# Performance work log

Measured on AMD Instinct MI355X. Metric: run time of the kernel, lower is better.

The kernel has to match this reference:

```python
import jax, jax.numpy as jnp
import numpy as np


def _construct_adj(adj, weight_cross_time):
    # adj: (N, N); weight_cross_time: (S-1, N, N) -> local_adj: (S*N, S*N)
    N = adj.shape[0]
    S = weight_cross_time.shape[0] + 1
    local_adj = jnp.zeros((S * N, S * N), dtype=adj.dtype)
    for i in range(S):  # diagonal blocks (small fixed loop over strides)
        local_adj = local_adj.at[i * N:(i + 1) * N, i * N:(i + 1) * N].set(adj)
    for k in range(S - 1):  # cross-time blocks, symmetric placement
        wk = weight_cross_time[k]
        local_adj = local_adj.at[k * N:(k + 1) * N, (k + 1) * N:(k + 2) * N].set(wk)
        local_adj = local_adj.at[(k + 1) * N:(k + 2) * N, k * N:(k + 1) * N].set(wk.T)
    return local_adj


def setup_inputs() -> dict:
    key = jax.random.key(0)
    k1, k2, k3, k4 = jax.random.split(key, 4)
    N, S, B, Cin, Cout = 1024, 3, 32, 64, 64
    # xavier_uniform-like scales for the learned adjacency parameters
    s_adj = float(np.sqrt(6.0 / (N + N)))
    x = jax.random.normal(k1, (S * N, B, Cin), dtype=jnp.float32)
    adj = jax.random.uniform(k2, (N, N), dtype=jnp.float32, minval=-s_adj, maxval=s_adj)
    weight_cross_time = jax.random.uniform(k3, (S - 1, N, N), dtype=jnp.float32, minval=-s_adj, maxval=s_adj)
    s_fc = float(np.sqrt(1.0 / Cin))
    W = jax.random.uniform(k4, (Cin, 2 * Cout), dtype=jnp.float32, minval=-s_fc, maxval=s_fc)
    b = jnp.zeros((2 * Cout,), dtype=jnp.float32)
    return {"x": x, "adj": adj, "weight_cross_time": weight_cross_time, "W": W, "b": b}


def reference(x, adj, weight_cross_time, W, b):
    # Faithful translation of gcn_operation.forward with activation='GLU'.
    Cout = W.shape[-1] // 2
    local_adj = _construct_adj(adj, weight_cross_time)          # (S*N, S*N)
    h = jnp.einsum('nm,mbc->nbc', local_adj, x)                  # (S*N, B, Cin)
    lhs_rhs = h @ W + b                                          # (S*N, B, 2*Cout)
    lhs, rhs = lhs_rhs[..., :Cout], lhs_rhs[..., Cout:]
    return lhs * jax.nn.sigmoid(rhs)                             # (S*N, B, Cout)
```

## Files before the change

### kernel.cpp

```cpp
#include <hip/hip_runtime.h>

typedef unsigned short u16;
typedef unsigned int   u32;
typedef __attribute__((ext_vector_type(8))) short short8;
typedef __attribute__((ext_vector_type(4))) float f32x4;

__device__ __forceinline__ u16 f2bf(float f) {
    u32 u = __float_as_uint(f);
    u = (u + 0x7fffu + ((u >> 16) & 1u)) >> 16;
    return (u16)u;
}

__device__ __forceinline__ void gld_lds16(const void* g, void* l) {
    __builtin_amdgcn_global_load_lds(
        (const __attribute__((address_space(1))) u32*)g,
        (__attribute__((address_space(3))) u32*)l, 16, 0, 0);
}

__global__ __launch_bounds__(256) void prep_kernel(
    const float* __restrict__ x, const float* __restrict__ adj,
    const float* __restrict__ wct, const float* __restrict__ W,
    u16* __restrict__ Ab, u16* __restrict__ W0T, u16* __restrict__ W1T,
    u16* __restrict__ Xt, u16* __restrict__ Wt)
{
    __shared__ float tile[64][65];
    const int t = threadIdx.x;
    const int bid = blockIdx.x;

    if (bid < 3072) {
        const int i4 = bid * 256 + t;
        const float4 v = (i4 < 262144) ? ((const float4*)adj)[i4]
                                       : ((const float4*)wct)[i4 - 262144];
        ushort4 o;
        o.x = f2bf(v.x); o.y = f2bf(v.y); o.z = f2bf(v.z); o.w = f2bf(v.w);
        ((ushort4*)Ab)[i4] = o;
        return;
    }

    const float* src; u16* dst; int C, R, r0, c0;
    if (bid < 3328)      { const int q = bid - 3072; src = wct;           dst = W0T; C = 1024; R = 1024; r0 = (q & 15) << 6; c0 = (q >> 4) << 6; }
    else if (bid < 3584) { const int q = bid - 3328; src = wct + 1048576; dst = W1T; C = 1024; R = 1024; r0 = (q & 15) << 6; c0 = (q >> 4) << 6; }
    else if (bid < 5120) { const int q = bid - 3584; src = x;             dst = Xt;  C = 2048; R = 3072; r0 = (q % 48) << 6; c0 = (q / 48) << 6; }
    else                 { const int q = bid - 5120; src = W;             dst = Wt;  C = 128;  R = 64;   r0 = 0;             c0 = q << 6; }

#pragma unroll
    for (int it = 0; it < 4; ++it) {
        const int f4 = it * 256 + t;
        const int r  = f4 >> 4;
        const int c4 = (f4 & 15) << 2;
        const float4 v = *(const float4*)&src[(size_t)(r0 + r) * C + c0 + c4];
        tile[r][c4]     = v.x; tile[r][c4 + 1] = v.y;
        tile[r][c4 + 2] = v.z; tile[r][c4 + 3] = v.w;
    }
    __syncthreads();
#pragma unroll
    for (int it = 0; it < 4; ++it) {
        const int f4 = it * 256 + t;
        const int u  = f4 >> 4;
        const int v4 = (f4 & 15) << 2;
        ushort4 o;
        o.x = f2bf(tile[v4][u]);     o.y = f2bf(tile[v4 + 1][u]);
        o.z = f2bf(tile[v4 + 2][u]); o.w = f2bf(tile[v4 + 3][u]);
        *(ushort4*)&dst[(size_t)(c0 + u) * R + r0 + v4] = o;
    }
}

__global__ __launch_bounds__(256, 3) void gemm_h_kernel(
    const u16* __restrict__ Ab,  const u16* __restrict__ W0b,
    const u16* __restrict__ W1b, const u16* __restrict__ W0T,
    const u16* __restrict__ W1T, const u16* __restrict__ Xt,
    const u16* __restrict__ Wt,  const float* __restrict__ bias,
    float* __restrict__ out)
{
    __shared__ u16 Adb[8192];
    __shared__ u16 Bdb[16384];
    __shared__ float Bias_sm[128];

    const int tid = threadIdx.x;
    const int bid = blockIdx.x;
    const int xcd = bid & 7;
    const int idx = bid >> 3;
    const int i   = idx >> 5;
    const int idp = idx & 31;
    const int row0 = (idp & 15) << 6;
    const int nt   = xcd * 2 + (idp >> 4);
    const int col0 = nt << 7;

    const int l    = tid & 63;
    const int w    = tid >> 6;
    const int wr   = ((tid >> 7) & 1) << 5;
    const int wc   = ((tid >> 6) & 1) << 6;
    const int lrow = l & 15;
    const int g16  = l >> 4;
    const int rsw  = lrow & 7;

    const int sub  = tid >> 3;
    const int srck = ((tid & 7) ^ (sub & 7)) << 3;
    const int wofs = w << 9;

    if (tid < 128) Bias_sm[tid] = bias[tid];

    u16 *Ac = Adb, *Ap = Adb + 4096, *Bc = Bdb, *Bp = Bdb + 8192;
    f32x4 acc[2][4] = {};

    auto stageA = [&](u16* dst, const u16* ta, int kel) {
        const u16* ga = ta + (size_t)sub * 1024 + kel + srck;
        gld_lds16(ga,             dst + wofs);
        gld_lds16(ga + 32 * 1024, dst + wofs + 2048);
    };
    auto stageB = [&](u16* dst, const u16* tb, int kel) {
        const u16* gb = tb + (size_t)sub * 3072 + kel + srck;
        gld_lds16(gb,             dst + wofs);
        gld_lds16(gb + 32 * 3072, dst + wofs + 2048);
        gld_lds16(gb + 64 * 3072, dst + wofs + 4096);
        gld_lds16(gb + 96 * 3072, dst + wofs + 6144);
    };
    auto step = [&](const u16* pfa, const u16* pfb, int kel, int do_pf) {
        __builtin_amdgcn_s_barrier();
        if (do_pf) {
            stageA(Ap, pfa, kel);
            stageB(Bp, pfb, kel);
            asm volatile("s_waitcnt vmcnt(6)" ::: "memory");
        } else {
            asm volatile("s_waitcnt vmcnt(0)" ::: "memory");
        }
        __builtin_amdgcn_s_barrier();

        short8 af[2][2], bfr[2][4];
#pragma unroll
        for (int kk = 0; kk < 2; ++kk) {
            const int so = (((kk << 2) | g16) ^ rsw) << 3;
#pragma unroll
            for (int fm = 0; fm < 2; ++fm)
                af[kk][fm] = *(const short8*)&Ac[(wr + fm * 16 + lrow) * 64 + so];
#pragma unroll
            for (int fn = 0; fn < 4; ++fn)
                bfr[kk][fn] = *(const short8*)&Bc[(wc + fn * 16 + lrow) * 64 + so];
        }
#pragma unroll
        for (int kk = 0; kk < 2; ++kk)
#pragma unroll
            for (int fm = 0; fm < 2; ++fm)
#pragma unroll
                for (int fn = 0; fn < 4; ++fn)
                    acc[fm][fn] = __builtin_amdgcn_mfma_f32_16x16x32_bf16(
                        af[kk][fm], bfr[kk][fn], acc[fm][fn], 0, 0, 0);
        u16* t;
        t = Ac; Ac = Ap; Ap = t;
        t = Bc; Bc = Bp; Bp = t;
    };
    auto run16 = [&](const u16* ta, const u16* tb,
                     const u16* na, const u16* nb, int hn) {
        for (int k = 1; k < 16; ++k) step(ta, tb, k << 6, 1);
        step(na, nb, 0, hn);
    };

    const size_t xbase = (size_t)col0 * 3072;
    const u16 *a0, *b0, *a1, *b1, *a2 = 0, *b2 = 0;
    int three = 0;
    if (i == 0) {
        a0 = Ab  + row0 * 1024; b0 = Xt + xbase;
        a1 = W0b + row0 * 1024; b1 = Xt + xbase + 1024;
    } else if (i == 1) {
        a0 = W0T + row0 * 1024; b0 = Xt + xbase;
        a1 = Ab  + row0 * 1024; b1 = Xt + xbase + 1024;
        a2 = W1b + row0 * 1024; b2 = Xt + xbase + 2048;
        three = 1;
    } else {
        a0 = W1T + row0 * 1024; b0 = Xt + xbase + 1024;
        a1 = Ab  + row0 * 1024; b1 = Xt + xbase + 2048;
    }

    stageA(Ac, a0, 0); stageB(Bc, b0, 0);
    run16(a0, b0, a1, b1, 1);
    if (three) { run16(a1, b1, a2, b2, 1); run16(a2, b2, 0, 0, 0); }
    else       { run16(a1, b1, 0, 0, 0); }

    __syncthreads();
    u16* Wsm = Adb;
    u16* Hsm = Bdb;
#pragma unroll
    for (int p = 0; p < 4; ++p)
        gld_lds16(Wt + (size_t)(p * 32 + sub) * 64 + srck,
                  Adb + p * 2048 + wofs);
#pragma unroll
    for (int fm = 0; fm < 2; ++fm)
#pragma unroll
        for (int fn = 0; fn < 4; ++fn)
#pragma unroll
            for (int r = 0; r < 4; ++r) {
                const int n   = wr + fm * 16 + (g16 << 2) + r;
                const int col = wc + fn * 16 + lrow;
                const int sl2 = ((col >> 3) ^ (n & 7));
                Hsm[n * 128 + (sl2 << 3) + (col & 7)] = f2bf(acc[fm][fn][r]);
            }
    __syncthreads();

    f32x4 acc2[2][8];
#pragma unroll
    for (int fm2 = 0; fm2 < 2; ++fm2)
#pragma unroll
        for (int fn = 0; fn < 8; ++fn) {
            const float bv = Bias_sm[fn * 16 + lrow];
            acc2[fm2][fn] = (f32x4){bv, bv, bv, bv};
        }
#pragma unroll
    for (int kk = 0; kk < 2; ++kk) {
        const int gg = (kk << 2) | g16;
        short8 ah[2], bw[8];
#pragma unroll
        for (int fm2 = 0; fm2 < 2; ++fm2) {
            const int rowp = (w << 5) + (fm2 << 4) + lrow;
            const int b = rowp >> 6, n = rowp & 63;
            const int sl2 = ((b << 3) | gg) ^ (n & 7);
            ah[fm2] = *(const short8*)&Hsm[n * 128 + (sl2 << 3)];
        }
#pragma unroll
        for (int fn = 0; fn < 8; ++fn) {
            const int c = (fn << 4) + lrow;
            const int sl2 = gg ^ (c & 7);
            bw[fn] = *(const short8*)&Wsm[c * 64 + (sl2 << 3)];
        }
#pragma unroll
        for (int fm2 = 0; fm2 < 2; ++fm2)
#pragma unroll
            for (int fn = 0; fn < 8; ++fn)
                acc2[fm2][fn] = __builtin_amdgcn_mfma_f32_16x16x32_bf16(
                    ah[fm2], bw[fn], acc2[fm2][fn], 0, 0, 0);
    }

    const int n0g = i * 1024 + row0;
    const int b0i = nt << 1;
#pragma unroll
    for (int fm2 = 0; fm2 < 2; ++fm2)
#pragma unroll
        for (int fn = 0; fn < 4; ++fn)
#pragma unroll
            for (int r = 0; r < 4; ++r) {
                const int rowp = (w << 5) + (fm2 << 4) + (g16 << 2) + r;
                const int b = rowp >> 6, nl = rowp & 63;
                const float lhs = acc2[fm2][fn][r];
                const float rhs = acc2[fm2][fn + 4][r];
                const float sg  = 1.0f / (1.0f + __expf(-rhs));
                const int c = (fn << 4) + lrow;
                out[((size_t)(n0g + nl) * 32 + (b0i + b)) * 64 + c] = lhs * sg;
            }
}

extern "C" void kernel_launch(void* const* d_in, const int* in_sizes, int n_in,
                              void* d_out, int out_size, void* d_ws, size_t ws_size,
                              hipStream_t stream)
{
    const float* x    = (const float*)d_in[0];
    const float* adj  = (const float*)d_in[1];
    const float* wct  = (const float*)d_in[2];
    const float* W    = (const float*)d_in[3];
    const float* bias = (const float*)d_in[4];
    float* out = (float*)d_out;

    char* ws = (char*)d_ws;
    u16* Xt  = (u16*)ws;
    u16* Ab  = (u16*)(ws + 12582912);
    u16* W0b = Ab + 1048576;
    u16* W1b = Ab + 2097152;
    u16* W0T = (u16*)(ws + 18874368);
    u16* W1T = W0T + 1048576;
    u16* Wt  = (u16*)(ws + 23068672);

    prep_kernel<<<5122, 256, 0, stream>>>(x, adj, wct, W, Ab, W0T, W1T, Xt, Wt);
    gemm_h_kernel<<<768, 256, 0, stream>>>(Ab, W0b, W1b, W0T, W1T, Xt, Wt, bias, out);
}
```

Before: 56.15 us.

## Fuse wct cast with transpose in prep and restructure GEMM pipeline barriers

The prep kernel now writes the plain bf16 copy of the cross-time weights from the same tiles it loads for the transposed copy, so wct is read from global memory once instead of twice and the grid shrinks. The GEMM main loop drops from two barriers per k-step to one. It now issues the prefetch, runs the MFMAs on the current buffer, then waits on vmcnt(0) and a barrier before swapping buffers, so loads overlap compute. The risk is that waiting on all outstanding loads at the end of each step exposes load latency when compute is short. Removing the __syncthreads before the epilogue depends on the barrier at the end of the last step.

```diff
diff --git a/kernel.cpp b/kernel.cpp
--- a/kernel.cpp
+++ b/kernel.cpp
@@ -27,21 +27,33 @@
     const int t = threadIdx.x;
     const int bid = blockIdx.x;
 
-    if (bid < 3072) {
+    if (bid < 1024) {
         const int i4 = bid * 256 + t;
-        const float4 v = (i4 < 262144) ? ((const float4*)adj)[i4]
-                                       : ((const float4*)wct)[i4 - 262144];
+        const float4 v = ((const float4*)adj)[i4];
         ushort4 o;
         o.x = f2bf(v.x); o.y = f2bf(v.y); o.z = f2bf(v.z); o.w = f2bf(v.w);
         ((ushort4*)Ab)[i4] = o;
         return;
     }
 
-    const float* src; u16* dst; int C, R, r0, c0;
-    if (bid < 3328)      { const int q = bid - 3072; src = wct;           dst = W0T; C = 1024; R = 1024; r0 = (q & 15) << 6; c0 = (q >> 4) << 6; }
-    else if (bid < 3584) { const int q = bid - 3328; src = wct + 1048576; dst = W1T; C = 1024; R = 1024; r0 = (q & 15) << 6; c0 = (q >> 4) << 6; }
-    else if (bid < 5120) { const int q = bid - 3584; src = x;             dst = Xt;  C = 2048; R = 3072; r0 = (q % 48) << 6; c0 = (q / 48) << 6; }
-    else                 { const int q = bid - 5120; src = W;             dst = Wt;  C = 128;  R = 64;   r0 = 0;             c0 = q << 6; }
+    const float* src; int C, R, r0, c0;
+    u16* dstT; u16* dstC = nullptr;
+    if (bid < 1536) {
+        const int q = bid - 1024;
+        const int mm = q >> 8, qq = q & 255;
+        src  = wct + (size_t)mm * 1048576;
+        dstT = mm ? W1T : W0T;
+        dstC = Ab + (size_t)(mm + 1) * 1048576;
+        C = 1024; R = 1024; r0 = (qq & 15) << 6; c0 = (qq >> 4) << 6;
+    } else if (bid < 3072) {
+        const int q = bid - 1536;
+        src = x; dstT = Xt; C = 2048; R = 3072;
+        r0 = (q % 48) << 6; c0 = (q / 48) << 6;
+    } else {
+        const int q = bid - 3072;
+        src = W; dstT = Wt; C = 128; R = 64;
+        r0 = 0; c0 = q << 6;
+    }
 
 #pragma unroll
     for (int it = 0; it < 4; ++it) {
@@ -51,6 +63,11 @@
         const float4 v = *(const float4*)&src[(size_t)(r0 + r) * C + c0 + c4];
         tile[r][c4]     = v.x; tile[r][c4 + 1] = v.y;
         tile[r][c4 + 2] = v.z; tile[r][c4 + 3] = v.w;
+        if (dstC) {
+            ushort4 o;
+            o.x = f2bf(v.x); o.y = f2bf(v.y); o.z = f2bf(v.z); o.w = f2bf(v.w);
+            *(ushort4*)&dstC[(size_t)(r0 + r) * 1024 + c0 + c4] = o;
+        }
     }
     __syncthreads();
 #pragma unroll
@@ -61,7 +78,7 @@
         ushort4 o;
         o.x = f2bf(tile[v4][u]);     o.y = f2bf(tile[v4 + 1][u]);
         o.z = f2bf(tile[v4 + 2][u]); o.w = f2bf(tile[v4 + 3][u]);
-        *(ushort4*)&dst[(size_t)(c0 + u) * R + r0 + v4] = o;
+        *(ushort4*)&dstT[(size_t)(c0 + u) * R + r0 + v4] = o;
     }
 }
 
@@ -116,15 +133,7 @@
         gld_lds16(gb + 96 * 3072, dst + wofs + 6144);
     };
     auto step = [&](const u16* pfa, const u16* pfb, int kel, int do_pf) {
-        __builtin_amdgcn_s_barrier();
-        if (do_pf) {
-            stageA(Ap, pfa, kel);
-            stageB(Bp, pfb, kel);
-            asm volatile("s_waitcnt vmcnt(6)" ::: "memory");
-        } else {
-            asm volatile("s_waitcnt vmcnt(0)" ::: "memory");
-        }
-        __builtin_amdgcn_s_barrier();
+        if (do_pf) { stageA(Ap, pfa, kel); stageB(Bp, pfb, kel); }
 
         short8 af[2][2], bfr[2][4];
 #pragma unroll
@@ -145,6 +154,9 @@
                 for (int fn = 0; fn < 4; ++fn)
                     acc[fm][fn] = __builtin_amdgcn_mfma_f32_16x16x32_bf16(
                         af[kk][fm], bfr[kk][fn], acc[fm][fn], 0, 0, 0);
+
+        asm volatile("s_waitcnt vmcnt(0)" ::: "memory");
+        __builtin_amdgcn_s_barrier();
         u16* t;
         t = Ac; Ac = Ap; Ap = t;
         t = Bc; Bc = Bp; Bp = t;
@@ -172,11 +184,13 @@
     }
 
     stageA(Ac, a0, 0); stageB(Bc, b0, 0);
+    asm volatile("s_waitcnt vmcnt(0)" ::: "memory");
+    __builtin_amdgcn_s_barrier();
+
     run16(a0, b0, a1, b1, 1);
     if (three) { run16(a1, b1, a2, b2, 1); run16(a2, b2, 0, 0, 0); }
     else       { run16(a1, b1, 0, 0, 0); }
 
-    __syncthreads();
     u16* Wsm = Adb;
     u16* Hsm = Bdb;
 #pragma unroll
@@ -267,6 +281,6 @@
     u16* W1T = W0T + 1048576;
     u16* Wt  = (u16*)(ws + 23068672);
 
-    prep_kernel<<<5122, 256, 0, stream>>>(x, adj, wct, W, Ab, W0T, W1T, Xt, Wt);
+    prep_kernel<<<3074, 256, 0, stream>>>(x, adj, wct, W, Ab, W0T, W1T, Xt, Wt);
     gemm_h_kernel<<<768, 256, 0, stream>>>(Ab, W0b, W1b, W0T, W1T, Xt, Wt, bias, out);
 }
```

New measurement: 56.04 us. Within noise of the previous version (-0.2%).
